# Optimization experiments

Measured on AMD Instinct MI355X. Metric: run time of the kernel, lower is better.

The kernel has to match this reference:

```python
import jax, jax.numpy as jnp
import numpy as np

HEAD_DIM = 64
NUM_FEATURES = 256


def _sample_orf(head_dim, num_features, seed=0):
    """Orthogonal random features with chi(d)-norm row scaling (FAVOR+)."""
    rng = np.random.RandomState(seed)
    blocks = []
    while len(blocks) * head_dim < num_features:
        G = rng.randn(head_dim, head_dim).astype(np.float32)
        Q, _ = np.linalg.qr(G)
        norms = np.linalg.norm(rng.randn(head_dim, head_dim).astype(np.float32), axis=1)
        blocks.append(np.diag(norms) @ Q.T)
    return np.concatenate(blocks, axis=0)[:num_features].astype(np.float32)


def _phi(x, omega, is_query):
    """FAVOR+ positive feature map with max-subtraction stabilization."""
    m = omega.shape[0]
    proj = jnp.einsum('bhnd,md->bhnm', x, omega)          # [B,H,N,M]
    norm = 0.5 * jnp.sum(x * x, axis=-1, keepdims=True)    # [B,H,N,1]
    log_phi = proj - norm
    if is_query:
        log_phi = log_phi - jnp.max(log_phi, axis=-1, keepdims=True)
    else:
        log_phi = log_phi - jnp.max(log_phi)
    return jnp.exp(log_phi) / np.float32(np.sqrt(m)) + 1e-4


def _causal_scan(phi_q, phi_k, v):
    """Causal linear-attention recurrence via lax.scan. States: S[B,H,M,D], z[B,H,M]."""
    B, H, N, M = phi_q.shape
    D = v.shape[-1]
    # seq-first for scan: [N,B,H,*]
    pq = jnp.moveaxis(phi_q, 2, 0)
    pk = jnp.moveaxis(phi_k, 2, 0)
    vt = jnp.moveaxis(v, 2, 0)

    S0 = jnp.zeros((B, H, M, D), dtype=phi_q.dtype)
    z0 = jnp.zeros((B, H, M), dtype=phi_q.dtype)

    def step(carry, xs):
        S, z = carry
        pq_i, pk_i, v_i = xs  # [B,H,M], [B,H,M], [B,H,D]
        S = S + pk_i[..., :, None] * v_i[..., None, :]
        z = z + pk_i
        num = jnp.einsum('bhm,bhmd->bhd', pq_i, S)
        den = jnp.sum(pq_i * z, axis=-1, keepdims=True) + 1e-6
        return (S, z), num / den

    _, out = jax.lax.scan(step, (S0, z0), (pq, pk, vt))  # out: [N,B,H,D]
    return jnp.moveaxis(out, 0, 2)


def setup_inputs() -> dict:
    key = jax.random.key(0)
    k1, k2, k3 = jax.random.split(key, 3)
    B, H, N, D = 2, 16, 4096, HEAD_DIM
    q = jax.random.normal(k1, (B, H, N, D), dtype=jnp.float32)
    k = jax.random.normal(k2, (B, H, N, D), dtype=jnp.float32)
    v = jax.random.normal(k3, (B, H, N, D), dtype=jnp.float32)
    omega = jnp.asarray(_sample_orf(HEAD_DIM, NUM_FEATURES))
    return {"q": q, "k": k, "v": v, "omega": omega}


def reference(q, k, v, omega):
    scale = q.shape[-1] ** (-0.25)
    phi_q = _phi(q * scale, omega, is_query=True)
    phi_k = _phi(k * scale, omega, is_query=False)
    # q_len == kv_len -> causal scan branch (matches original forward)
    out = _causal_scan(phi_q.astype(jnp.float32), phi_k.astype(jnp.float32),
                       v.astype(jnp.float32))
    return out.astype(q.dtype)
```

## Files before the change

kernel.cpp:

```cpp
#include <hip/hip_runtime.h>
#include <cstddef>

#define BH    32
#define NSEQ  4096
#define MFEAT 256
#define CHUNK 128
#define NCH   32
#define SROW  65
#define SPITCH (SROW*256)

#define SCALE 0.35355339059327373f

typedef unsigned int uint_t;
typedef _Float16 half_t;
typedef __attribute__((ext_vector_type(8))) _Float16 half8;
typedef __attribute__((ext_vector_type(4))) float f32x4;

__device__ __forceinline__ f32x4 mfma16(half8 a, half8 b, f32x4 c) {
  return __builtin_amdgcn_mfma_f32_16x16x32_f16(a, b, c, 0, 0, 0);
}
__device__ __forceinline__ uint_t enc_f(float x) {
  uint_t u = __float_as_uint(x);
  return (u & 0x80000000u) ? ~u : (u | 0x80000000u);
}
__device__ __forceinline__ float dec_f(uint_t u) {
  u = (u & 0x80000000u) ? (u ^ 0x80000000u) : ~u;
  return __uint_as_float(u);
}
__device__ __forceinline__ half8 cvt_h8(float4 a, float4 b) {
  half8 h;
  h[0] = (half_t)a.x; h[1] = (half_t)a.y; h[2] = (half_t)a.z; h[3] = (half_t)a.w;
  h[4] = (half_t)b.x; h[5] = (half_t)b.y; h[6] = (half_t)b.z; h[7] = (half_t)b.w;
  return h;
}

__global__ void k_init(uint_t* kmax) { *kmax = enc_f(-__builtin_inff()); }

__global__ __launch_bounds__(256, 2) void k_maxes4(
    const float* __restrict__ q, const float* __restrict__ kx,
    const float* __restrict__ omega, uint_t* __restrict__ kmax,
    half_t* __restrict__ phiQ, float* __restrict__ hnKg)
{
  __shared__ half_t Wl[256 * 64];
  __shared__ float nrm[64];
  __shared__ float red[4];

  const int tid = threadIdx.x;
  const int lane = tid & 63;
  const int w = tid >> 6;
  const int lc = lane & 15, rg = lane >> 4, koff = rg * 8;
  const int swz = (lc & 7) << 3;
  const size_t rowbase = (size_t)blockIdx.x * 64;

  for (int l = tid; l < 2048; l += 256) {
    int m = l >> 3, d8 = (l & 7) * 8;
    float4 a = *(const float4*)(omega + m * 64 + d8);
    float4 b = *(const float4*)(omega + m * 64 + d8 + 4);
    *(half8*)&Wl[m * 64 + (d8 ^ ((m & 7) << 3))] = cvt_h8(a, b);
  }
  half8 aq[2], akf[2];
  {
    const float* qp = q + (rowbase + w * 16 + lc) * 64 + koff;
    const float* kp = kx + (rowbase + w * 16 + lc) * 64 + koff;
    float pn = 0.f;
    #pragma unroll
    for (int ks = 0; ks < 2; ks++) {
      float4 a = *(const float4*)(qp + ks * 32);
      float4 b = *(const float4*)(qp + ks * 32 + 4);
      a.x *= SCALE; a.y *= SCALE; a.z *= SCALE; a.w *= SCALE;
      b.x *= SCALE; b.y *= SCALE; b.z *= SCALE; b.w *= SCALE;
      aq[ks] = cvt_h8(a, b);
      float4 c = *(const float4*)(kp + ks * 32);
      float4 d = *(const float4*)(kp + ks * 32 + 4);
      c.x *= SCALE; c.y *= SCALE; c.z *= SCALE; c.w *= SCALE;
      d.x *= SCALE; d.y *= SCALE; d.z *= SCALE; d.w *= SCALE;
      pn += c.x * c.x + c.y * c.y + c.z * c.z + c.w * c.w
          + d.x * d.x + d.y * d.y + d.z * d.z + d.w * d.w;
      akf[ks] = cvt_h8(c, d);
    }
    pn += __shfl_xor(pn, 16, 64);
    pn += __shfl_xor(pn, 32, 64);
    if (rg == 0) {
      nrm[w * 16 + lc] = 0.5f * pn;
      hnKg[rowbase + w * 16 + lc] = 0.5f * pn;
    }
  }
  __syncthreads();

  {
    f32x4 acck[16];
    #pragma unroll
    for (int ct = 0; ct < 16; ct++) acck[ct] = (f32x4){0.f, 0.f, 0.f, 0.f};
    #pragma unroll
    for (int ks = 0; ks < 2; ks++)
      #pragma unroll
      for (int ct = 0; ct < 16; ct++) {
        half8 b = *(const half8*)&Wl[(ct * 16 + lc) * 64 + ((ks * 32 + koff) ^ swz)];
        acck[ct] = mfma16(akf[ks], b, acck[ct]);
      }
    float hn[4];
    #pragma unroll
    for (int r = 0; r < 4; r++) hn[r] = nrm[w * 16 + rg * 4 + r];
    float bm = -3.4e38f;
    #pragma unroll
    for (int ct = 0; ct < 16; ct++)
      #pragma unroll
      for (int r = 0; r < 4; r++) bm = fmaxf(bm, acck[ct][r] - hn[r]);
    #pragma unroll
    for (int off = 1; off < 64; off <<= 1) bm = fmaxf(bm, __shfl_xor(bm, off, 64));
    if (lane == 0) red[w] = bm;
  }

  f32x4 acc[16];
  #pragma unroll
  for (int ct = 0; ct < 16; ct++) acc[ct] = (f32x4){0.f, 0.f, 0.f, 0.f};
  #pragma unroll
  for (int ks = 0; ks < 2; ks++)
    #pragma unroll
    for (int ct = 0; ct < 16; ct++) {
      half8 b = *(const half8*)&Wl[(ct * 16 + lc) * 64 + ((ks * 32 + koff) ^ swz)];
      acc[ct] = mfma16(aq[ks], b, acc[ct]);
    }
  float rowm[4];
  #pragma unroll
  for (int r = 0; r < 4; r++) {
    float m0 = -3.4e38f;
    #pragma unroll
    for (int ct = 0; ct < 16; ct++) m0 = fmaxf(m0, acc[ct][r]);
    m0 = fmaxf(m0, __shfl_xor(m0, 1, 64));
    m0 = fmaxf(m0, __shfl_xor(m0, 2, 64));
    m0 = fmaxf(m0, __shfl_xor(m0, 4, 64));
    m0 = fmaxf(m0, __shfl_xor(m0, 8, 64));
    rowm[r] = m0;
  }
  #pragma unroll
  for (int ct = 0; ct < 16; ct++)
    #pragma unroll
    for (int r = 0; r < 4; r++)
      acc[ct][r] = __expf(acc[ct][r] - rowm[r]) * 0.0625f + 1e-4f;

  __syncthreads();
  if (tid == 0)
    atomicMax(kmax, enc_f(fmaxf(fmaxf(red[0], red[1]), fmaxf(red[2], red[3]))));

  half_t* st = Wl;
  #pragma unroll
  for (int hh = 0; hh < 2; hh++) {
    if (hh) __syncthreads();
    #pragma unroll
    for (int c8 = 0; c8 < 8; c8++)
      #pragma unroll
      for (int r = 0; r < 4; r++)
        st[(w * 16 + rg * 4 + r) * 136 + c8 * 16 + lc] = (half_t)acc[hh * 8 + c8][r];
    __syncthreads();
    #pragma unroll
    for (int e = 0; e < 4; e++) {
      int l = tid + e * 256;
      int row = l >> 4, c = (l & 15) * 8;
      *(half8*)(phiQ + (rowbase + row) * 256 + hh * 128 + c) =
          *(const half8*)&st[row * 136 + c];
    }
  }
}

__global__ __launch_bounds__(256, 2) void k_state4(
    const float* __restrict__ kx, const float* __restrict__ v,
    const float* __restrict__ omega, const float* __restrict__ hnKg,
    const uint_t* __restrict__ kmax, half_t* __restrict__ spA,
    half_t* __restrict__ phiKg)
{
  __shared__ half_t WP[256 * 64];
  __shared__ half_t vt[80 * 128];

  const int tid = threadIdx.x;
  const int lane = tid & 63;
  const int w = tid >> 6;
  const int lc = lane & 15, rg = lane >> 4, koff = rg * 8;
  const int wr = w * 32;
  const int swz = (lc & 7) << 3;
  const int blk = blockIdx.x;
  const size_t nbase = (size_t)(blk >> 5) * NSEQ + (size_t)(blk & 31) * CHUNK;
  const float gmaxv = dec_f(*kmax);

  for (int l = tid; l < 2048; l += 256) {
    int m = l >> 3, d8 = (l & 7) * 8;
    float4 a = *(const float4*)(omega + m * 64 + d8);
    float4 b = *(const float4*)(omega + m * 64 + d8 + 4);
    *(half8*)&WP[m * 64 + (d8 ^ ((m & 7) << 3))] = cvt_h8(a, b);
  }
  for (int l = tid; l < 2048; l += 256) {
    int j = l >> 4, dq = (l & 15) * 4;
    float4 vv = *(const float4*)(v + (nbase + j) * 64 + dq);
    vt[(dq + 0) * 128 + (j ^ (((dq + 0) & 7) << 3))] = (half_t)vv.x;
    vt[(dq + 1) * 128 + (j ^ (((dq + 1) & 7) << 3))] = (half_t)vv.y;
    vt[(dq + 2) * 128 + (j ^ (((dq + 2) & 7) << 3))] = (half_t)vv.z;
    vt[(dq + 3) * 128 + (j ^ (((dq + 3) & 7) << 3))] = (half_t)vv.w;
  }
  if (tid < 128) vt[64 * 128 + tid] = (half_t)1.0f;

  half8 ak[2][2];
  float hnr[2][4];
  #pragma unroll
  for (int rt = 0; rt < 2; rt++) {
    const float* kp = kx + (nbase + wr + rt * 16 + lc) * 64 + koff;
    #pragma unroll
    for (int ks = 0; ks < 2; ks++) {
      float4 a = *(const float4*)(kp + ks * 32);
      float4 b = *(const float4*)(kp + ks * 32 + 4);
      a.x *= SCALE; a.y *= SCALE; a.z *= SCALE; a.w *= SCALE;
      b.x *= SCALE; b.y *= SCALE; b.z *= SCALE; b.w *= SCALE;
      ak[rt][ks] = cvt_h8(a, b);
    }
    #pragma unroll
    for (int r = 0; r < 4; r++)
      hnr[rt][r] = hnKg[nbase + wr + rt * 16 + rg * 4 + r];
  }
  __syncthreads();

  f32x4 accP[2][16];
  #pragma unroll
  for (int rt = 0; rt < 2; rt++)
    #pragma unroll
    for (int ct = 0; ct < 16; ct++) accP[rt][ct] = (f32x4){0.f, 0.f, 0.f, 0.f};
  #pragma unroll
  for (int ks = 0; ks < 2; ks++)
    #pragma unroll
    for (int ct = 0; ct < 16; ct++) {
      half8 b = *(const half8*)&WP[(ct * 16 + lc) * 64 + ((ks * 32 + koff) ^ swz)];
      accP[0][ct] = mfma16(ak[0][ks], b, accP[0][ct]);
      accP[1][ct] = mfma16(ak[1][ks], b, accP[1][ct]);
    }
  #pragma unroll
  for (int rt = 0; rt < 2; rt++)
    #pragma unroll
    for (int ct = 0; ct < 16; ct++)
      #pragma unroll
      for (int r = 0; r < 4; r++)
        accP[rt][ct][r] = __expf(accP[rt][ct][r] - hnr[rt][r] - gmaxv) * 0.0625f + 1e-4f;

  half_t* pkT = WP;
  #pragma unroll
  for (int h = 0; h < 2; h++) {
    __syncthreads();
    #pragma unroll
    for (int rt = 0; rt < 2; rt++)
      #pragma unroll
      for (int c8 = 0; c8 < 8; c8++) {
        int m = c8 * 16 + lc;
        int ct = h * 8 + c8;
        #pragma unroll
        for (int r = 0; r < 4; r++) {
          int j = wr + rt * 16 + rg * 4 + r;
          pkT[m * 128 + (j ^ ((m & 7) << 3))] = (half_t)accP[rt][ct][r];
        }
      }
    __syncthreads();
    f32x4 acc2[5][2];
    #pragma unroll
    for (int rt = 0; rt < 5; rt++) {
      acc2[rt][0] = (f32x4){0.f, 0.f, 0.f, 0.f};
      acc2[rt][1] = (f32x4){0.f, 0.f, 0.f, 0.f};
    }
    #pragma unroll
    for (int ks = 0; ks < 4; ks++) {
      half8 b0 = *(const half8*)&pkT[((2 * w + 0) * 16 + lc) * 128 + ((ks * 32 + koff) ^ swz)];
      half8 b1 = *(const half8*)&pkT[((2 * w + 1) * 16 + lc) * 128 + ((ks * 32 + koff) ^ swz)];
      #pragma unroll
      for (int rt = 0; rt < 5; rt++) {
        half8 a = *(const half8*)&vt[(rt * 16 + lc) * 128 + ((ks * 32 + koff) ^ swz)];
        acc2[rt][0] = mfma16(a, b0, acc2[rt][0]);
        acc2[rt][1] = mfma16(a, b1, acc2[rt][1]);
      }
    }
    #pragma unroll
    for (int rt = 0; rt < 5; rt++)
      #pragma unroll
      for (int c2 = 0; c2 < 2; c2++)
        #pragma unroll
        for (int r = 0; r < 4; r++) {
          int row = rt * 16 + rg * 4 + r;
          if (row < SROW)
            spA[(size_t)blk * SPITCH + row * 256 + h * 128 + (2 * w + c2) * 16 + lc] =
                (half_t)acc2[rt][c2][r];
        }
  }

  half_t* PhS = WP;
  #pragma unroll
  for (int hh = 0; hh < 2; hh++) {
    __syncthreads();
    #pragma unroll
    for (int rt = 0; rt < 2; rt++)
      #pragma unroll
      for (int c8 = 0; c8 < 8; c8++)
        #pragma unroll
        for (int r = 0; r < 4; r++) {
          int j = wr + rt * 16 + rg * 4 + r;
          PhS[j * 128 + ((c8 * 16 + lc) ^ ((j & 7) << 3))] =
              (half_t)accP[rt][hh * 8 + c8][r];
        }
    __syncthreads();
    #pragma unroll
    for (int e = 0; e < 8; e++) {
      int l = tid + e * 256;
      int j = l >> 4, c8b = (l & 15) * 8;
      *(half8*)(phiKg + (nbase + j) * 256 + hh * 128 + c8b) =
          *(const half8*)&PhS[j * 128 + (c8b ^ ((j & 7) << 3))];
    }
  }
}

__global__ __launch_bounds__(256) void k_prefix(
    const uint_t* __restrict__ spA, uint_t* __restrict__ spB)
{
  int r = blockIdx.x * 256 + threadIdx.x;
  if (r >= SPITCH / 2) return;
  int bh = blockIdx.y;
  const uint_t* src = spA + (size_t)bh * NCH * (SPITCH / 2) + r;
  uint_t* dst = spB + (size_t)bh * NCH * (SPITCH / 2) + r;
  float r0 = 0.f, r1 = 0.f;
  for (int c = 0; c < NCH; c++) {
    union { uint_t u; half_t h[2]; } cv, ov;
    cv.u = src[(size_t)c * (SPITCH / 2)];
    ov.h[0] = (half_t)r0; ov.h[1] = (half_t)r1;
    dst[(size_t)c * (SPITCH / 2)] = ov.u;
    r0 += (float)cv.h[0];
    r1 += (float)cv.h[1];
  }
}

__global__ __launch_bounds__(512) void k_attn8(
    const half_t* __restrict__ phiQ, const half_t* __restrict__ phiK,
    const float* __restrict__ v, const half_t* __restrict__ spB,
    float* __restrict__ out)
{
  __shared__ half_t sm[18432];
  half_t* PQ  = sm;
  half_t* SST = sm + 8192;
  half_t* AS  = sm;
  half_t* VT  = sm + 8192;

  const int tid = threadIdx.x;
  const int lane = tid & 63;
  const int w = tid >> 6;
  const int lc = lane & 15, rg = lane >> 4, koff = rg * 8;
  const int blk = blockIdx.x;
  const size_t nbase = (size_t)(blk >> 5) * NSEQ + (size_t)(blk & 31) * CHUNK;
  const half_t* spb = spB + (size_t)blk * SPITCH;
  const int swz = (lc & 7) << 3;

  f32x4 accA[8], accO[5];
  #pragma unroll
  for (int it = 0; it < 8; it++) accA[it] = (f32x4){0.f, 0.f, 0.f, 0.f};
  #pragma unroll
  for (int cs = 0; cs < 5; cs++) accO[cs] = (f32x4){0.f, 0.f, 0.f, 0.f};

  for (int mt = 0; mt < 4; mt++) {
    if (mt) __syncthreads();
    #pragma unroll
    for (int e = 0; e < 2; e++) {
      int l = tid + e * 512;
      int ro = l >> 3, c8 = (l & 7) * 8;
      *(half8*)&PQ[ro * 64 + (c8 ^ ((ro & 7) << 3))] =
          *(const half8*)(phiQ + (nbase + ro) * 256 + mt * 64 + c8);
    }
    { int ro = tid >> 3, c8 = (tid & 7) * 8;
      if (tid < 520)
        *(half8*)&SST[ro * 64 + (c8 ^ ((ro & 7) << 3))] =
            *(const half8*)(spb + ro * 256 + mt * 64 + c8); }
    if (tid < 8) { int l = tid + 512; int ro = l >> 3, c8 = (l & 7) * 8;
      *(half8*)&SST[ro * 64 + (c8 ^ ((ro & 7) << 3))] =
          *(const half8*)(spb + ro * 256 + mt * 64 + c8); }
    half8 af0 = *(const half8*)(phiK + (nbase + w * 16 + lc) * 256 + mt * 64 + koff);
    half8 af1 = *(const half8*)(phiK + (nbase + w * 16 + lc) * 256 + mt * 64 + 32 + koff);
    __syncthreads();
    #pragma unroll
    for (int ks2 = 0; ks2 < 64; ks2 += 32) {
      half8 a = ks2 ? af1 : af0;
      int sA = (ks2 + koff) ^ swz;
      half8 bO = *(const half8*)&PQ[(w * 16 + lc) * 64 + sA];
      #pragma unroll
      for (int it = 0; it < 8; it++) {
        half8 b = *(const half8*)&PQ[(it * 16 + lc) * 64 + sA];
        accA[it] = mfma16(a, b, accA[it]);
      }
      #pragma unroll
      for (int cs = 0; cs < 5; cs++) {
        half8 as_ = *(const half8*)&SST[(cs * 16 + lc) * 64 + sA];
        accO[cs] = mfma16(as_, bO, accO[cs]);
      }
    }
  }
  __syncthreads();

  #pragma unroll
  for (int e = 0; e < 4; e++) {
    int l = tid + e * 512;
    int j = l >> 4, dq = (l & 15) * 4;
    float4 vv = *(const float4*)(v + (nbase + j) * 64 + dq);
    VT[(dq + 0) * 128 + (j ^ (((dq + 0) & 7) << 3))] = (half_t)vv.x;
    VT[(dq + 1) * 128 + (j ^ (((dq + 1) & 7) << 3))] = (half_t)vv.y;
    VT[(dq + 2) * 128 + (j ^ (((dq + 2) & 7) << 3))] = (half_t)vv.z;
    VT[(dq + 3) * 128 + (j ^ (((dq + 3) & 7) << 3))] = (half_t)vv.w;
  }
  if (tid < 128) VT[64 * 128 + tid] = (half_t)1.0f;

  #pragma unroll
  for (int h = 0; h < 2; h++) {
    if ((w >> 2) == h) {
      #pragma unroll
      for (int it = 0; it < 8; it++) {
        int i = it * 16 + lc;
        #pragma unroll
        for (int r = 0; r < 4; r++) {
          int j = w * 16 + rg * 4 + r;
          float val = (j <= i) ? accA[it][r] : 0.f;
          AS[i * 64 + ((j - h * 64) ^ ((i & 7) << 3))] = (half_t)val;
        }
      }
    }
    __syncthreads();
    #pragma unroll
    for (int ks2 = 0; ks2 < 64; ks2 += 32) {
      int sj = (ks2 + koff) ^ swz;
      half8 b = *(const half8*)&AS[(w * 16 + lc) * 64 + sj];
      #pragma unroll
      for (int cs = 0; cs < 5; cs++) {
        half8 a = *(const half8*)&VT[(cs * 16 + lc) * 128 + ((h * 64 + ks2 + koff) ^ swz)];
        accO[cs] = mfma16(a, b, accO[cs]);
      }
    }
    __syncthreads();
  }

  float den = __shfl(accO[4][0], lane & 15, 64) + 1e-6f;
  float inv = 1.0f / den;
  float* OS = (float*)sm;
  #pragma unroll
  for (int cs = 0; cs < 4; cs++)
    #pragma unroll
    for (int r = 0; r < 4; r++)
      OS[(w * 16 + lc) * 68 + cs * 16 + rg * 4 + r] = accO[cs][r] * inv;
  __syncthreads();
  #pragma unroll
  for (int e = 0; e < 4; e++) {
    int l = tid + e * 512;
    int row = l >> 4, c4 = (l & 15) * 4;
    *(float4*)(out + (nbase + row) * 64 + c4) = *(const float4*)&OS[row * 68 + c4];
  }
}

extern "C" void kernel_launch(void* const* d_in, const int* in_sizes, int n_in,
                              void* d_out, int out_size, void* d_ws, size_t ws_size,
                              hipStream_t stream) {
  const float* q = (const float*)d_in[0];
  const float* k = (const float*)d_in[1];
  const float* v = (const float*)d_in[2];
  const float* omega = (const float*)d_in[3];
  float* out = (float*)d_out;
  char* ws = (char*)d_ws;

  float*  hnKg = (float*)(ws + 0);
  half_t* spB  = (half_t*)(ws + 524288);
  half_t* phiQ = (half_t*)(ws + 34603008);
  half_t* phiK = (half_t*)(ws + 101711872);
  half_t* spA  = (half_t*)(ws + 168820736);
  uint_t* kmax = (uint_t*)(ws + 202899456);

  k_init<<<1, 1, 0, stream>>>(kmax);
  k_maxes4<<<2048, 256, 0, stream>>>(q, k, omega, kmax, phiQ, hnKg);
  k_state4<<<1024, 256, 0, stream>>>(k, v, omega, hnKg, kmax, spA, phiK);
  k_prefix<<<dim3(33, 32), 256, 0, stream>>>((const uint_t*)spA, (uint_t*)spB);
  k_attn8<<<1024, 512, 0, stream>>>(phiQ, phiK, v, spB, out);
}
```

Before: 154.6 us.

## Split phi kernel into separate Q/K blocks and halve feature dim per state block

The first kernel now launches twice as many blocks, each handling either the query feature map or the key max/norm, instead of one block doing both. The state kernel splits the 256 features into two halves across blocks, which shrinks accumulators and shared memory (one aliased buffer) and doubles the grid. The goal is more parallelism and occupancy and less register pressure. The cost is redundant omega staging and reloading the k and v chunk in both half-blocks.

```diff
diff --git a/kernel.cpp b/kernel.cpp
--- a/kernel.cpp
+++ b/kernel.cpp
@@ -36,7 +36,7 @@
 
 __global__ void k_init(uint_t* kmax) { *kmax = enc_f(-__builtin_inff()); }
 
-__global__ __launch_bounds__(256, 2) void k_maxes4(
+__global__ __launch_bounds__(256, 2) void k_phi1(
     const float* __restrict__ q, const float* __restrict__ kx,
     const float* __restrict__ omega, uint_t* __restrict__ kmax,
     half_t* __restrict__ phiQ, float* __restrict__ hnKg)
@@ -50,7 +50,8 @@
   const int w = tid >> 6;
   const int lc = lane & 15, rg = lane >> 4, koff = rg * 8;
   const int swz = (lc & 7) << 3;
-  const size_t rowbase = (size_t)blockIdx.x * 64;
+  const bool qpath = (blockIdx.x < 2048);
+  const size_t rowbase = (size_t)(qpath ? blockIdx.x : (blockIdx.x - 2048)) * 64;
 
   for (int l = tid; l < 2048; l += 256) {
     int m = l >> 3, d8 = (l & 7) * 8;
@@ -58,45 +59,99 @@
     float4 b = *(const float4*)(omega + m * 64 + d8 + 4);
     *(half8*)&Wl[m * 64 + (d8 ^ ((m & 7) << 3))] = cvt_h8(a, b);
   }
-  half8 aq[2], akf[2];
-  {
-    const float* qp = q + (rowbase + w * 16 + lc) * 64 + koff;
-    const float* kp = kx + (rowbase + w * 16 + lc) * 64 + koff;
-    float pn = 0.f;
-    #pragma unroll
-    for (int ks = 0; ks < 2; ks++) {
-      float4 a = *(const float4*)(qp + ks * 32);
-      float4 b = *(const float4*)(qp + ks * 32 + 4);
-      a.x *= SCALE; a.y *= SCALE; a.z *= SCALE; a.w *= SCALE;
-      b.x *= SCALE; b.y *= SCALE; b.z *= SCALE; b.w *= SCALE;
-      aq[ks] = cvt_h8(a, b);
-      float4 c = *(const float4*)(kp + ks * 32);
-      float4 d = *(const float4*)(kp + ks * 32 + 4);
-      c.x *= SCALE; c.y *= SCALE; c.z *= SCALE; c.w *= SCALE;
-      d.x *= SCALE; d.y *= SCALE; d.z *= SCALE; d.w *= SCALE;
-      pn += c.x * c.x + c.y * c.y + c.z * c.z + c.w * c.w
-          + d.x * d.x + d.y * d.y + d.z * d.z + d.w * d.w;
-      akf[ks] = cvt_h8(c, d);
-    }
-    pn += __shfl_xor(pn, 16, 64);
-    pn += __shfl_xor(pn, 32, 64);
-    if (rg == 0) {
-      nrm[w * 16 + lc] = 0.5f * pn;
-      hnKg[rowbase + w * 16 + lc] = 0.5f * pn;
-    }
-  }
-  __syncthreads();
-
-  {
-    f32x4 acck[16];
-    #pragma unroll
-    for (int ct = 0; ct < 16; ct++) acck[ct] = (f32x4){0.f, 0.f, 0.f, 0.f};
+
+  if (qpath) {
+    half8 aq[2];
+    {
+      const float* qp = q + (rowbase + w * 16 + lc) * 64 + koff;
+      #pragma unroll
+      for (int ks = 0; ks < 2; ks++) {
+        float4 a = *(const float4*)(qp + ks * 32);
+        float4 b = *(const float4*)(qp + ks * 32 + 4);
+        a.x *= SCALE; a.y *= SCALE; a.z *= SCALE; a.w *= SCALE;
+        b.x *= SCALE; b.y *= SCALE; b.z *= SCALE; b.w *= SCALE;
+        aq[ks] = cvt_h8(a, b);
+      }
+    }
+    __syncthreads();
+    f32x4 acc[16];
+    #pragma unroll
+    for (int ct = 0; ct < 16; ct++) acc[ct] = (f32x4){0.f, 0.f, 0.f, 0.f};
     #pragma unroll
     for (int ks = 0; ks < 2; ks++)
       #pragma unroll
       for (int ct = 0; ct < 16; ct++) {
         half8 b = *(const half8*)&Wl[(ct * 16 + lc) * 64 + ((ks * 32 + koff) ^ swz)];
-        acck[ct] = mfma16(akf[ks], b, acck[ct]);
+        acc[ct] = mfma16(aq[ks], b, acc[ct]);
+      }
+    float rowm[4];
+    #pragma unroll
+    for (int r = 0; r < 4; r++) {
+      float m0 = -3.4e38f;
+      #pragma unroll
+      for (int ct = 0; ct < 16; ct++) m0 = fmaxf(m0, acc[ct][r]);
+      m0 = fmaxf(m0, __shfl_xor(m0, 1, 64));
+      m0 = fmaxf(m0, __shfl_xor(m0, 2, 64));
+      m0 = fmaxf(m0, __shfl_xor(m0, 4, 64));
+      m0 = fmaxf(m0, __shfl_xor(m0, 8, 64));
+      rowm[r] = m0;
+    }
+    #pragma unroll
+    for (int ct = 0; ct < 16; ct++)
+      #pragma unroll
+      for (int r = 0; r < 4; r++)
+        acc[ct][r] = __expf(acc[ct][r] - rowm[r]) * 0.0625f + 1e-4f;
+
+    half_t* st = Wl;
+    #pragma unroll
+    for (int hh = 0; hh < 2; hh++) {
+      __syncthreads();
+      #pragma unroll
+      for (int c8 = 0; c8 < 8; c8++)
+        #pragma unroll
+        for (int r = 0; r < 4; r++)
+          st[(w * 16 + rg * 4 + r) * 136 + c8 * 16 + lc] = (half_t)acc[hh * 8 + c8][r];
+      __syncthreads();
+      #pragma unroll
+      for (int e = 0; e < 4; e++) {
+        int l = tid + e * 256;
+        int row = l >> 4, c = (l & 15) * 8;
+        *(half8*)(phiQ + (rowbase + row) * 256 + hh * 128 + c) =
+            *(const half8*)&st[row * 136 + c];
+      }
+    }
+  } else {
+    half8 akf[2];
+    {
+      const float* kp = kx + (rowbase + w * 16 + lc) * 64 + koff;
+      float pn = 0.f;
+      #pragma unroll
+      for (int ks = 0; ks < 2; ks++) {
+        float4 c = *(const float4*)(kp + ks * 32);
+        float4 d = *(const float4*)(kp + ks * 32 + 4);
+        c.x *= SCALE; c.y *= SCALE; c.z *= SCALE; c.w *= SCALE;
+        d.x *= SCALE; d.y *= SCALE; d.z *= SCALE; d.w *= SCALE;
+        pn += c.x * c.x + c.y * c.y + c.z * c.z + c.w * c.w
+            + d.x * d.x + d.y * d.y + d.z * d.z + d.w * d.w;
+        akf[ks] = cvt_h8(c, d);
+      }
+      pn += __shfl_xor(pn, 16, 64);
+      pn += __shfl_xor(pn, 32, 64);
+      if (rg == 0) {
+        nrm[w * 16 + lc] = 0.5f * pn;
+        hnKg[rowbase + w * 16 + lc] = 0.5f * pn;
+      }
+    }
+    __syncthreads();
+    f32x4 acc[16];
+    #pragma unroll
+    for (int ct = 0; ct < 16; ct++) acc[ct] = (f32x4){0.f, 0.f, 0.f, 0.f};
+    #pragma unroll
+    for (int ks = 0; ks < 2; ks++)
+      #pragma unroll
+      for (int ct = 0; ct < 16; ct++) {
+        half8 b = *(const half8*)&Wl[(ct * 16 + lc) * 64 + ((ks * 32 + koff) ^ swz)];
+        acc[ct] = mfma16(akf[ks], b, acc[ct]);
       }
     float hn[4];
     #pragma unroll
@@ -105,72 +160,27 @@
     #pragma unroll
     for (int ct = 0; ct < 16; ct++)
       #pragma unroll
-      for (int r = 0; r < 4; r++) bm = fmaxf(bm, acck[ct][r] - hn[r]);
+      for (int r = 0; r < 4; r++) bm = fmaxf(bm, acc[ct][r] - hn[r]);
     #pragma unroll
     for (int off = 1; off < 64; off <<= 1) bm = fmaxf(bm, __shfl_xor(bm, off, 64));
     if (lane == 0) red[w] = bm;
-  }
-
-  f32x4 acc[16];
-  #pragma unroll
-  for (int ct = 0; ct < 16; ct++) acc[ct] = (f32x4){0.f, 0.f, 0.f, 0.f};
-  #pragma unroll
-  for (int ks = 0; ks < 2; ks++)
-    #pragma unroll
-    for (int ct = 0; ct < 16; ct++) {
-      half8 b = *(const half8*)&Wl[(ct * 16 + lc) * 64 + ((ks * 32 + koff) ^ swz)];
-      acc[ct] = mfma16(aq[ks], b, acc[ct]);
-    }
-  float rowm[4];
-  #pragma unroll
-  for (int r = 0; r < 4; r++) {
-    float m0 = -3.4e38f;
-    #pragma unroll
-    for (int ct = 0; ct < 16; ct++) m0 = fmaxf(m0, acc[ct][r]);
-    m0 = fmaxf(m0, __shfl_xor(m0, 1, 64));
-    m0 = fmaxf(m0, __shfl_xor(m0, 2, 64));
-    m0 = fmaxf(m0, __shfl_xor(m0, 4, 64));
-    m0 = fmaxf(m0, __shfl_xor(m0, 8, 64));
-    rowm[r] = m0;
-  }
-  #pragma unroll
-  for (int ct = 0; ct < 16; ct++)
-    #pragma unroll
-    for (int r = 0; r < 4; r++)
-      acc[ct][r] = __expf(acc[ct][r] - rowm[r]) * 0.0625f + 1e-4f;
-
-  __syncthreads();
-  if (tid == 0)
-    atomicMax(kmax, enc_f(fmaxf(fmaxf(red[0], red[1]), fmaxf(red[2], red[3]))));
-
-  half_t* st = Wl;
-  #pragma unroll
-  for (int hh = 0; hh < 2; hh++) {
-    if (hh) __syncthreads();
-    #pragma unroll
-    for (int c8 = 0; c8 < 8; c8++)
-      #pragma unroll
-      for (int r = 0; r < 4; r++)
-        st[(w * 16 + rg * 4 + r) * 136 + c8 * 16 + lc] = (half_t)acc[hh * 8 + c8][r];
-    __syncthreads();
-    #pragma unroll
-    for (int e = 0; e < 4; e++) {
-      int l = tid + e * 256;
-      int row = l >> 4, c = (l & 15) * 8;
-      *(half8*)(phiQ + (rowbase + row) * 256 + hh * 128 + c) =
-          *(const half8*)&st[row * 136 + c];
-    }
-  }
-}
-
-__global__ __launch_bounds__(256, 2) void k_state4(
+    __syncthreads();
+    if (tid == 0)
+      atomicMax(kmax, enc_f(fmaxf(fmaxf(red[0], red[1]), fmaxf(red[2], red[3]))));
+  }
+}
+
+__global__ __launch_bounds__(256, 2) void k_state5(
     const float* __restrict__ kx, const float* __restrict__ v,
     const float* __restrict__ omega, const float* __restrict__ hnKg,
     const uint_t* __restrict__ kmax, half_t* __restrict__ spA,
     half_t* __restrict__ phiKg)
 {
-  __shared__ half_t WP[256 * 64];
-  __shared__ half_t vt[80 * 128];
+  __shared__ half_t sm[18432];
+  half_t* Wl  = sm;
+  half_t* pkT = sm;
+  half_t* PhS = sm;
+  half_t* vt  = sm + 8192;
 
   const int tid = threadIdx.x;
   const int lane = tid & 63;
@@ -178,15 +188,17 @@
   const int lc = lane & 15, rg = lane >> 4, koff = rg * 8;
   const int wr = w * 32;
   const int swz = (lc & 7) << 3;
-  const int blk = blockIdx.x;
+  const int mh = blockIdx.x & 1;
+  const int blk = blockIdx.x >> 1;
   const size_t nbase = (size_t)(blk >> 5) * NSEQ + (size_t)(blk & 31) * CHUNK;
   const float gmaxv = dec_f(*kmax);
 
-  for (int l = tid; l < 2048; l += 256) {
+  for (int l = tid; l < 1024; l += 256) {
     int m = l >> 3, d8 = (l & 7) * 8;
-    float4 a = *(const float4*)(omega + m * 64 + d8);
-    float4 b = *(const float4*)(omega + m * 64 + d8 + 4);
-    *(half8*)&WP[m * 64 + (d8 ^ ((m & 7) << 3))] = cvt_h8(a, b);
+    const float* op = omega + (mh * 128 + m) * 64 + d8;
+    float4 a = *(const float4*)(op);
+    float4 b = *(const float4*)(op + 4);
+    *(half8*)&Wl[m * 64 + (d8 ^ ((m & 7) << 3))] = cvt_h8(a, b);
   }
   for (int l = tid; l < 2048; l += 256) {
     int j = l >> 4, dq = (l & 15) * 4;
@@ -217,95 +229,86 @@
   }
   __syncthreads();
 
-  f32x4 accP[2][16];
+  f32x4 accP[2][8];
   #pragma unroll
   for (int rt = 0; rt < 2; rt++)
     #pragma unroll
-    for (int ct = 0; ct < 16; ct++) accP[rt][ct] = (f32x4){0.f, 0.f, 0.f, 0.f};
+    for (int ct = 0; ct < 8; ct++) accP[rt][ct] = (f32x4){0.f, 0.f, 0.f, 0.f};
   #pragma unroll
   for (int ks = 0; ks < 2; ks++)
     #pragma unroll
-    for (int ct = 0; ct < 16; ct++) {
-      half8 b = *(const half8*)&WP[(ct * 16 + lc) * 64 + ((ks * 32 + koff) ^ swz)];
+    for (int ct = 0; ct < 8; ct++) {
+      half8 b = *(const half8*)&Wl[(ct * 16 + lc) * 64 + ((ks * 32 + koff) ^ swz)];
       accP[0][ct] = mfma16(ak[0][ks], b, accP[0][ct]);
       accP[1][ct] = mfma16(ak[1][ks], b, accP[1][ct]);
     }
   #pragma unroll
   for (int rt = 0; rt < 2; rt++)
     #pragma unroll
-    for (int ct = 0; ct < 16; ct++)
+    for (int ct = 0; ct < 8; ct++)
       #pragma unroll
       for (int r = 0; r < 4; r++)
         accP[rt][ct][r] = __expf(accP[rt][ct][r] - hnr[rt][r] - gmaxv) * 0.0625f + 1e-4f;
 
-  half_t* pkT = WP;
-  #pragma unroll
-  for (int h = 0; h < 2; h++) {
+  #pragma unroll
+  for (int ms = 0; ms < 2; ms++) {
     __syncthreads();
     #pragma unroll
     for (int rt = 0; rt < 2; rt++)
       #pragma unroll
-      for (int c8 = 0; c8 < 8; c8++) {
-        int m = c8 * 16 + lc;
-        int ct = h * 8 + c8;
+      for (int c4 = 0; c4 < 4; c4++) {
+        int msub = c4 * 16 + lc;
+        int ct = ms * 4 + c4;
         #pragma unroll
         for (int r = 0; r < 4; r++) {
           int j = wr + rt * 16 + rg * 4 + r;
-          pkT[m * 128 + (j ^ ((m & 7) << 3))] = (half_t)accP[rt][ct][r];
+          pkT[msub * 128 + (j ^ ((msub & 7) << 3))] = (half_t)accP[rt][ct][r];
         }
       }
     __syncthreads();
-    f32x4 acc2[5][2];
-    #pragma unroll
-    for (int rt = 0; rt < 5; rt++) {
-      acc2[rt][0] = (f32x4){0.f, 0.f, 0.f, 0.f};
-      acc2[rt][1] = (f32x4){0.f, 0.f, 0.f, 0.f};
-    }
+    f32x4 acc2[5];
+    #pragma unroll
+    for (int rt = 0; rt < 5; rt++) acc2[rt] = (f32x4){0.f, 0.f, 0.f, 0.f};
     #pragma unroll
     for (int ks = 0; ks < 4; ks++) {
-      half8 b0 = *(const half8*)&pkT[((2 * w + 0) * 16 + lc) * 128 + ((ks * 32 + koff) ^ swz)];
-      half8 b1 = *(const half8*)&pkT[((2 * w + 1) * 16 + lc) * 128 + ((ks * 32 + koff) ^ swz)];
+      half8 b = *(const half8*)&pkT[(w * 16 + lc) * 128 + ((ks * 32 + koff) ^ swz)];
       #pragma unroll
       for (int rt = 0; rt < 5; rt++) {
         half8 a = *(const half8*)&vt[(rt * 16 + lc) * 128 + ((ks * 32 + koff) ^ swz)];
-        acc2[rt][0] = mfma16(a, b0, acc2[rt][0]);
-        acc2[rt][1] = mfma16(a, b1, acc2[rt][1]);
+        acc2[rt] = mfma16(a, b, acc2[rt]);
       }
     }
     #pragma unroll
     for (int rt = 0; rt < 5; rt++)
       #pragma unroll
-      for (int c2 = 0; c2 < 2; c2++)
-        #pragma unroll
-        for (int r = 0; r < 4; r++) {
-          int row = rt * 16 + rg * 4 + r;
-          if (row < SROW)
-            spA[(size_t)blk * SPITCH + row * 256 + h * 128 + (2 * w + c2) * 16 + lc] =
-                (half_t)acc2[rt][c2][r];
-        }
-  }
-
-  half_t* PhS = WP;
-  #pragma unroll
-  for (int hh = 0; hh < 2; hh++) {
+      for (int r = 0; r < 4; r++) {
+        int row = rt * 16 + rg * 4 + r;
+        if (row < SROW)
+          spA[(size_t)blk * SPITCH + row * 256 + mh * 128 + ms * 64 + w * 16 + lc] =
+              (half_t)acc2[rt][r];
+      }
+  }
+
+  #pragma unroll
+  for (int ms = 0; ms < 2; ms++) {
     __syncthreads();
     #pragma unroll
     for (int rt = 0; rt < 2; rt++)
       #pragma unroll
-      for (int c8 = 0; c8 < 8; c8++)
+      for (int c4 = 0; c4 < 4; c4++)
         #pragma unroll
         for (int r = 0; r < 4; r++) {
           int j = wr + rt * 16 + rg * 4 + r;
-          PhS[j * 128 + ((c8 * 16 + lc) ^ ((j & 7) << 3))] =
-              (half_t)accP[rt][hh * 8 + c8][r];
+          int msub = c4 * 16 + lc;
+          PhS[j * 64 + (msub ^ ((j & 7) << 3))] = (half_t)accP[rt][ms * 4 + c4][r];
         }
     __syncthreads();
     #pragma unroll
-    for (int e = 0; e < 8; e++) {
+    for (int e = 0; e < 4; e++) {
       int l = tid + e * 256;
-      int j = l >> 4, c8b = (l & 15) * 8;
-      *(half8*)(phiKg + (nbase + j) * 256 + hh * 128 + c8b) =
-          *(const half8*)&PhS[j * 128 + (c8b ^ ((j & 7) << 3))];
+      int j = l >> 3, c8 = (l & 7) * 8;
+      *(half8*)(phiKg + (nbase + j) * 256 + mh * 128 + ms * 64 + c8) =
+          *(const half8*)&PhS[j * 64 + (c8 ^ ((j & 7) << 3))];
     }
   }
 }
@@ -468,8 +471,8 @@
   uint_t* kmax = (uint_t*)(ws + 202899456);
 
   k_init<<<1, 1, 0, stream>>>(kmax);
-  k_maxes4<<<2048, 256, 0, stream>>>(q, k, omega, kmax, phiQ, hnKg);
-  k_state4<<<1024, 256, 0, stream>>>(k, v, omega, hnKg, kmax, spA, phiK);
+  k_phi1<<<4096, 256, 0, stream>>>(q, k, omega, kmax, phiQ, hnKg);
+  k_state5<<<2048, 256, 0, stream>>>(k, v, omega, hnKg, kmax, spA, phiK);
   k_prefix<<<dim3(33, 32), 256, 0, stream>>>((const uint_t*)spA, (uint_t*)spB);
   k_attn8<<<1024, 512, 0, stream>>>(phiQ, phiK, v, spB, out);
 }
```

Measured after the change: 159.8 us. 3.4% more time.
